# Kernel optimization log

Measured on AMD Instinct MI355X. Metric: run time of the kernel, lower is better.

The kernel has to match this reference:

```python
import jax, jax.numpy as jnp
import numpy as np

LN2 = float(np.log(2.0))
CUTOFF_L = 0.5


def _ssp(x):
    # shifted softplus: log(0.5*exp(x) + 0.5)
    return jax.nn.softplus(x) - LN2


def _pair_idx(n):
    # ordered pairs arranged [n, n-1]: for each i, all j != i
    idx = np.arange(n)
    j = np.stack([np.concatenate([idx[:k], idx[k + 1:]]) for k in range(n)])  # [n, n-1]
    i = np.broadcast_to(idx[:, None], j.shape)
    return jnp.asarray(i), jnp.asarray(j)


def _mlp3(x, w1, b1, w2, b2, w3, b3):
    h = _ssp(x @ w1 + b1)
    h = _ssp(h @ w2 + b2)
    return h @ w3 + b3


def _backflow_cutoff(r, L=CUTOFF_L):
    r = r / L
    return jnp.where(r < L, r ** 2 * (6.0 - 8.0 * r + 3.0 * r ** 2), jnp.ones((), r.dtype))


def setup_inputs() -> dict:
    key = jax.random.key(0)
    ks = jax.random.split(key, 12)
    B, N, D, K = 512, 32, 256, 8
    dims_e = [D, 40, 6, 1]
    dims_n = [D, 81, 25, 8]

    def lin(k, fi, fo):
        return jax.random.normal(k, (fi, fo), jnp.float32) / np.sqrt(fi)

    inp = {
        'rs': jax.random.normal(ks[0], (B, N, 3), jnp.float32),
        'xs': jax.random.normal(ks[1], (B, N, D), jnp.float32),
        'coords': jax.random.normal(ks[2], (K, 3), jnp.float32) * 2.0,
        'ew1': lin(ks[3], dims_e[0], dims_e[1]), 'eb1': jnp.zeros((dims_e[1],), jnp.float32),
        'ew2': lin(ks[4], dims_e[1], dims_e[2]), 'eb2': jnp.zeros((dims_e[2],), jnp.float32),
        'ew3': lin(ks[5], dims_e[2], dims_e[3]), 'eb3': jnp.zeros((dims_e[3],), jnp.float32),
        'nw1': lin(ks[6], dims_n[0], dims_n[1]), 'nb1': jnp.zeros((dims_n[1],), jnp.float32),
        'nw2': lin(ks[7], dims_n[1], dims_n[2]), 'nb2': jnp.zeros((dims_n[2],), jnp.float32),
        'nw3': lin(ks[8], dims_n[2], dims_n[3]), 'nb3': jnp.zeros((dims_n[3],), jnp.float32),
    }
    return inp


def reference(rs, xs, coords, ew1, eb1, ew2, eb2, ew3, eb3,
              nw1, nb1, nw2, nb2, nw3, nb3):
    n_elec = rs.shape[-2]
    i, j = _pair_idx(n_elec)  # [n, n-1] static index arrays

    # electron-electron backflow
    diffs_elec = rs[..., i, :] - rs[..., j, :]                    # [B, n, n-1, 3]
    pair_feat = xs[..., i, :] * xs[..., j, :]                     # [B, n, n-1, D]
    w_pair = _mlp3(pair_feat, ew1, eb1, ew2, eb2, ew3, eb3)       # [B, n, n-1, 1]
    bf_elec = (w_pair * diffs_elec).sum(axis=-2)                  # [B, n, 3]

    # electron-nucleus backflow
    diffs_nuc = rs[..., :, None, :] - coords                      # [B, n, K, 3]
    w_nuc = _mlp3(xs, nw1, nb1, nw2, nb2, nw3, nb3)               # [B, n, K]
    bf_nuc = (w_nuc[..., None] * diffs_nuc).sum(axis=-2)          # [B, n, 3]

    dist_nuc = jnp.linalg.norm(diffs_nuc, axis=-1)                # [B, n, K]
    cutoff = _backflow_cutoff(dist_nuc).prod(axis=-1)             # [B, n]

    return rs + 1e-4 * cutoff[..., None] * (bf_elec + bf_nuc)
```

## Files before the change

kernel.cpp:

```cpp
#include <hip/hip_runtime.h>
#include <stdint.h>

static constexpr int B_ = 512, N_ = 32, D_ = 256, K_ = 8;
static constexpr int E1 = 40, E2 = 6;
static constexpr int N1 = 81, N2 = 25, N3 = 8;
static constexpr int XBP = 264;
static constexpr int H1P = 72;
static constexpr int HEP = 96;
static constexpr int EWT = 264;
static constexpr int TKP = 48;
static constexpr int NWP = 104;
static constexpr int TILE16 = 16 * TKP;
static constexpr float LN2f  = 0.69314718055994530942f;
static constexpr float L2Ef  = 1.44269504088896340736f;

typedef float    f32x4 __attribute__((ext_vector_type(4)));
typedef _Float16 f16x8 __attribute__((ext_vector_type(8)));

__device__ __forceinline__ float sspf(float x) {
    float t = __builtin_amdgcn_exp2f(x * L2Ef);
    return LN2f * __builtin_amdgcn_logf(fmaf(t, 0.5f, 0.5f));
}

__global__ __launch_bounds__(512) void k_fused(
    const float* __restrict__ rs, const float* __restrict__ xs,
    const float* __restrict__ coords,
    const float* __restrict__ ew1, const float* __restrict__ eb1,
    const float* __restrict__ ew2, const float* __restrict__ eb2,
    const float* __restrict__ ew3, const float* __restrict__ eb3,
    const float* __restrict__ nw1, const float* __restrict__ nb1,
    const float* __restrict__ nw2, const float* __restrict__ nb2,
    const float* __restrict__ nw3, const float* __restrict__ nb3,
    float* __restrict__ out)
{
    __shared__ alignas(16) _Float16 xs_h[N_ * XBP];
    __shared__ alignas(16) _Float16 wbuf[E1 * EWT];
    __shared__ alignas(16) char uni[18688];
    __shared__ float nw3_s[N2 * N3];
    __shared__ float rs_s[N_ * 3];
    __shared__ float nb2_s[N2];
    __shared__ float nb3_s[N3];
    __shared__ float co_s[K_ * 3];
    __shared__ float bfn_s[N_ * 3];
    __shared__ float cut_s[N_];
    __shared__ float bfe_s[N_ * 3];

    _Float16* h1e  = (_Float16*)(uni + 9216);
    float*    h2e  = (float*)(uni + 15360);
    _Float16* nw2T = (_Float16*)uni;

    const int b = blockIdx.x, t = threadIdx.x;
    const int wv = t >> 6, l = t & 63, quad = l >> 4, c = l & 15;

    f16x8 b2f[2];
    #pragma unroll
    for (int Kt = 0; Kt < 2; ++Kt) {
        union { uint32_t d[4]; f16x8 v; } f;
        #pragma unroll
        for (int d2 = 0; d2 < 4; ++d2) {
            int k0 = Kt * 32 + quad * 8 + 2 * d2;
            union { _Float16 h[2]; uint32_t u; } pk;
            pk.h[0] = (_Float16)((k0 < E1 && c < E2) ? ew2[k0 * E2 + c] : 0.f);
            pk.h[1] = (_Float16)((k0 + 1 < E1 && c < E2) ? ew2[(k0 + 1) * E2 + c] : 0.f);
            f.d[d2] = pk.u;
        }
        b2f[Kt] = f.v;
    }
    float eb1v[3];
    #pragma unroll
    for (int Nt = 0; Nt < 3; ++Nt) { int n = Nt * 16 + c; eb1v[Nt] = (n < E1) ? eb1[n] : 0.f; }
    const float eb2v = (c < E2) ? eb2[c] : 0.f;
    const float w3v  = (c < E2) ? ew3[c] : 0.f;
    const float eb3v = eb3[0];

    {
        const float4* src = (const float4*)(xs + (size_t)b * N_ * D_);
        #pragma unroll
        for (int u = 0; u < 4; ++u) {
            int q = t + 512 * u;
            float4 v = src[q];
            int row = q >> 6, col4 = q & 63;
            union { _Float16 h[4]; uint64_t u64; } pk;
            pk.h[0] = (_Float16)v.x; pk.h[1] = (_Float16)v.y;
            pk.h[2] = (_Float16)v.z; pk.h[3] = (_Float16)v.w;
            *(uint64_t*)&xs_h[row * XBP + col4 * 4] = pk.u64;
        }
    }
    {
        const float4* src = (const float4*)ew1;
        #pragma unroll
        for (int u = 0; u < 5; ++u) {
            int q = t + 512 * u;
            float4 v = src[q];
            int k = q / 10, n0 = (q - 10 * k) * 4;
            wbuf[(n0 + 0) * EWT + k] = (_Float16)v.x;
            wbuf[(n0 + 1) * EWT + k] = (_Float16)v.y;
            wbuf[(n0 + 2) * EWT + k] = (_Float16)v.z;
            wbuf[(n0 + 3) * EWT + k] = (_Float16)v.w;
        }
    }
    if (t < 128) {
        int m = t >> 2, q4 = t & 3;
        *(uint64_t*)(uni + 9216 + m * (HEP * 2) + 160 + q4 * 8) = 0ull;
    }
    if (t < N_ * 3) rs_s[t] = rs[b * N_ * 3 + t];
    if (t < N2 * N3) nw3_s[t] = nw3[t];
    if (t < N2) nb2_s[t] = nb2[t];
    if (t < N3) nb3_s[t] = nb3[t];
    if (t < K_ * 3) co_s[t] = coords[t];
    __syncthreads();

    if (wv < 6) {
        _Float16* tile = (_Float16*)uni + wv * TILE16;
        const int ln = l & 15, lq = l >> 4;
        const int gn = wv * 16 + ln;
        const bool gok = (gn < N1);
        const int n_col = wv * 16 + c;
        const float nb1v = (n_col < N1) ? nb1[n_col] : 0.f;

        float pf[8];
        #pragma unroll
        for (int u = 0; u < 8; ++u)
            pf[u] = gok ? nw1[(lq + 4 * u) * N1 + gn] : 0.f;

        f32x4 acc[2];
        acc[0] = (f32x4){0.f, 0.f, 0.f, 0.f};
        acc[1] = (f32x4){0.f, 0.f, 0.f, 0.f};

        #pragma unroll 1
        for (int Kt = 0; Kt < 8; ++Kt) {
            #pragma unroll
            for (int u = 0; u < 8; ++u)
                tile[ln * TKP + lq + 4 * u] = (_Float16)pf[u];
            if (Kt < 7) {
                const float* wk = nw1 + (Kt + 1) * 32 * N1 + gn;
                #pragma unroll
                for (int u = 0; u < 8; ++u)
                    pf[u] = gok ? wk[(lq + 4 * u) * N1] : 0.f;
            }
            f16x8 Bf = *(const f16x8*)&tile[c * TKP + quad * 8];
            #pragma unroll
            for (int Mt = 0; Mt < 2; ++Mt) {
                f16x8 A = *(const f16x8*)&xs_h[(Mt * 16 + c) * XBP + Kt * 32 + quad * 8];
                acc[Mt] = __builtin_amdgcn_mfma_f32_16x16x32_f16(A, Bf, acc[Mt], 0, 0, 0);
            }
        }
        if (n_col < N1) {
            #pragma unroll
            for (int Mt = 0; Mt < 2; ++Mt)
                #pragma unroll
                for (int r2 = 0; r2 < 4; ++r2) {
                    int m = Mt * 16 + quad * 4 + r2;
                    h1e[m * HEP + n_col] = (_Float16)sspf(acc[Mt][r2] + nb1v);
                }
        }
    }
    __syncthreads();

    f16x8 b1f[3][8];
    #pragma unroll
    for (int Nt = 0; Nt < 3; ++Nt) {
        int n = Nt * 16 + c;
        bool ok = (n < E1);
        int row = ok ? n : 0;
        #pragma unroll
        for (int Kt = 0; Kt < 8; ++Kt) {
            f16x8 v = *(const f16x8*)&wbuf[row * EWT + Kt * 32 + quad * 8];
            if (!ok) v = (f16x8)(_Float16)0.f;
            b1f[Nt][Kt] = v;
        }
    }
    #pragma unroll
    for (int u = 0; u < 6; ++u) {
        int idx = t + 512 * u;
        int n = idx / 96, kk = idx - 96 * n;
        float v = (kk < N1 && n < N2) ? nw2[kk * N2 + n] : 0.f;
        nw2T[n * NWP + kk] = (_Float16)v;
    }
    __syncthreads();

    if (wv < 4) {
        const int Mt = wv & 1, Nt = wv >> 1;
        f32x4 acc2 = {0.f, 0.f, 0.f, 0.f};
        #pragma unroll
        for (int Kt2 = 0; Kt2 < 3; ++Kt2) {
            f16x8 A  = *(const f16x8*)&h1e[(Mt * 16 + c) * HEP + Kt2 * 32 + quad * 8];
            f16x8 Bf = *(const f16x8*)&nw2T[(Nt * 16 + c) * NWP + Kt2 * 32 + quad * 8];
            acc2 = __builtin_amdgcn_mfma_f32_16x16x32_f16(A, Bf, acc2, 0, 0, 0);
        }
        int n = Nt * 16 + c;
        if (n < N2) {
            #pragma unroll
            for (int r2 = 0; r2 < 4; ++r2) {
                int m = Mt * 16 + quad * 4 + r2;
                h2e[m * 26 + n] = sspf(acc2[r2] + nb2_s[n]);
            }
        }
    }
    __syncthreads();

    if (t < 256) {
        const int r = t >> 3, s = t & 7;
        float w = nb3_s[s];
        const int rb = r * 26;
        #pragma unroll
        for (int kk = 0; kk < N2; ++kk)
            w = fmaf(h2e[rb + kk], nw3_s[kk * N3 + s], w);

        float dx = rs_s[r * 3 + 0] - co_s[s * 3 + 0];
        float dy = rs_s[r * 3 + 1] - co_s[s * 3 + 1];
        float dz = rs_s[r * 3 + 2] - co_s[s * 3 + 2];
        float cx = w * dx, cy = w * dy, cz = w * dz;
        #pragma unroll
        for (int m2 = 1; m2 < 8; m2 <<= 1) {
            cx += __shfl_xor(cx, m2);
            cy += __shfl_xor(cy, m2);
            cz += __shfl_xor(cz, m2);
        }
        float rr  = sqrtf(dx * dx + dy * dy + dz * dz);
        float xsc = 2.f * rr;
        float cf  = (xsc < 0.5f) ? xsc * xsc * (6.f - 8.f * xsc + 3.f * xsc * xsc) : 1.f;
        #pragma unroll
        for (int m2 = 1; m2 < 8; m2 <<= 1) cf *= __shfl_xor(cf, m2);
        if (s == 0) {
            bfn_s[r * 3 + 0] = cx;
            bfn_s[r * 3 + 1] = cy;
            bfn_s[r * 3 + 2] = cz;
            cut_s[r] = cf;
        }
    }
    __syncthreads();

    _Float16* myh1 = (_Float16*)(uni + wv * (16 * H1P * 2));
    *(uint64_t*)&myh1[c * H1P + 48 + quad * 4] = 0ull;

    #pragma unroll 1
    for (int q8 = 0; q8 < 4; ++q8) {
        const int i = wv + 8 * q8;
        f32x4 acc[2][3];
        #pragma unroll
        for (int h = 0; h < 2; ++h)
            #pragma unroll
            for (int Nt = 0; Nt < 3; ++Nt) acc[h][Nt] = (f32x4){0.f, 0.f, 0.f, 0.f};

        #pragma unroll
        for (int Kt = 0; Kt < 8; ++Kt) {
            const int koff = Kt * 32 + quad * 8;
            f16x8 iv  = *(const f16x8*)&xs_h[i * XBP + koff];
            f16x8 jv0 = *(const f16x8*)&xs_h[c * XBP + koff];
            f16x8 jv1 = *(const f16x8*)&xs_h[(16 + c) * XBP + koff];
            f16x8 A0 = iv * jv0;
            f16x8 A1 = iv * jv1;
            #pragma unroll
            for (int Nt = 0; Nt < 3; ++Nt) {
                acc[0][Nt] = __builtin_amdgcn_mfma_f32_16x16x32_f16(A0, b1f[Nt][Kt], acc[0][Nt], 0, 0, 0);
                acc[1][Nt] = __builtin_amdgcn_mfma_f32_16x16x32_f16(A1, b1f[Nt][Kt], acc[1][Nt], 0, 0, 0);
            }
        }

        const float rix = rs_s[i * 3 + 0], riy = rs_s[i * 3 + 1], riz = rs_s[i * 3 + 2];
        float cxi = 0.f, cyi = 0.f, czi = 0.f;
        #pragma unroll
        for (int h = 0; h < 2; ++h) {
            #pragma unroll
            for (int Nt = 0; Nt < 3; ++Nt) {
                #pragma unroll
                for (int r2 = 0; r2 < 4; ++r2) {
                    float hv = sspf(acc[h][Nt][r2] + eb1v[Nt]);
                    myh1[(quad * 4 + r2) * H1P + Nt * 16 + c] = (_Float16)hv;
                }
            }
            f32x4 acc2 = {0.f, 0.f, 0.f, 0.f};
            #pragma unroll
            for (int Kt2 = 0; Kt2 < 2; ++Kt2) {
                f16x8 a2 = *(const f16x8*)&myh1[c * H1P + Kt2 * 32 + quad * 8];
                acc2 = __builtin_amdgcn_mfma_f32_16x16x32_f16(a2, b2f[Kt2], acc2, 0, 0, 0);
            }
            float wp[4];
            #pragma unroll
            for (int r2 = 0; r2 < 4; ++r2) wp[r2] = sspf(acc2[r2] + eb2v) * w3v;
            #pragma unroll
            for (int m2 = 1; m2 < 16; m2 <<= 1) {
                #pragma unroll
                for (int r2 = 0; r2 < 4; ++r2) wp[r2] += __shfl_xor(wp[r2], m2);
            }
            #pragma unroll
            for (int r2 = 0; r2 < 4; ++r2) {
                int j = quad * 4 + r2 + 16 * h;
                float wj = wp[r2] + eb3v;
                cxi = fmaf(wj, rix - rs_s[j * 3 + 0], cxi);
                cyi = fmaf(wj, riy - rs_s[j * 3 + 1], cyi);
                czi = fmaf(wj, riz - rs_s[j * 3 + 2], czi);
            }
        }
        #pragma unroll
        for (int m2 = 16; m2 < 64; m2 <<= 1) {
            cxi += __shfl_xor(cxi, m2);
            cyi += __shfl_xor(cyi, m2);
            czi += __shfl_xor(czi, m2);
        }
        if (l == 0) {
            bfe_s[i * 3 + 0] = cxi;
            bfe_s[i * 3 + 1] = cyi;
            bfe_s[i * 3 + 2] = czi;
        }
    }
    __syncthreads();

    if (t < N_ * 3) {
        int i = t / 3;
        out[(size_t)b * (N_ * 3) + t] =
            rs_s[t] + 1e-4f * cut_s[i] * (bfe_s[t] + bfn_s[t]);
    }
}

extern "C" void kernel_launch(void* const* d_in, const int* in_sizes, int n_in,
                              void* d_out, int out_size, void* d_ws, size_t ws_size,
                              hipStream_t stream)
{
    const float* rs     = (const float*)d_in[0];
    const float* xs     = (const float*)d_in[1];
    const float* coords = (const float*)d_in[2];
    const float* ew1    = (const float*)d_in[3];
    const float* eb1    = (const float*)d_in[4];
    const float* ew2    = (const float*)d_in[5];
    const float* eb2    = (const float*)d_in[6];
    const float* ew3    = (const float*)d_in[7];
    const float* eb3    = (const float*)d_in[8];
    const float* nw1    = (const float*)d_in[9];
    const float* nb1    = (const float*)d_in[10];
    const float* nw2    = (const float*)d_in[11];
    const float* nb2    = (const float*)d_in[12];
    const float* nw3    = (const float*)d_in[13];
    const float* nb3    = (const float*)d_in[14];

    k_fused<<<B_, 512, 0, stream>>>(rs, xs, coords, ew1, eb1, ew2, eb2, ew3, eb3,
                                    nw1, nb1, nw2, nb2, nw3, nb3, (float*)d_out);
}
```

Baseline: 133.8 us.

## Transpose edge MLP MFMAs to chain layers in registers and fold log2 scaling

The edge-MLP first-layer MFMA now has its operands swapped, so each lane's accumulator holds hidden units for one pair column. That output can feed the second layer directly as a 16x16x16 MFMA B-operand, with no LDS round trip through a per-wave h1 buffer. The ln2/log2e factors of the shifted softplus are folded into weights and biases, so each activation skips two multiplies. Biases are preloaded into the accumulators, and the final reduction becomes two cross-quad shuffles. The barrier before the pair loop and the LDS staging are removed, at the cost of slightly different fp16 rounding from the scaled weights.

```diff
diff --git a/kernel.cpp b/kernel.cpp
--- a/kernel.cpp
+++ b/kernel.cpp
@@ -5,7 +5,6 @@
 static constexpr int E1 = 40, E2 = 6;
 static constexpr int N1 = 81, N2 = 25, N3 = 8;
 static constexpr int XBP = 264;
-static constexpr int H1P = 72;
 static constexpr int HEP = 96;
 static constexpr int EWT = 264;
 static constexpr int TKP = 48;
@@ -16,10 +15,17 @@
 
 typedef float    f32x4 __attribute__((ext_vector_type(4)));
 typedef _Float16 f16x8 __attribute__((ext_vector_type(8)));
-
-__device__ __forceinline__ float sspf(float x) {
-    float t = __builtin_amdgcn_exp2f(x * L2Ef);
-    return LN2f * __builtin_amdgcn_logf(fmaf(t, 0.5f, 0.5f));
+typedef _Float16 f16x4 __attribute__((ext_vector_type(4)));
+
+#if __has_builtin(__builtin_amdgcn_mfma_f32_16x16x16_f16)
+#define MFMA16(A, B, C) __builtin_amdgcn_mfma_f32_16x16x16_f16((A), (B), (C), 0, 0, 0)
+#else
+#define MFMA16(A, B, C) __builtin_amdgcn_mfma_f32_16x16x16f16((A), (B), (C), 0, 0, 0)
+#endif
+
+__device__ __forceinline__ float ssp2(float t) {
+    float e = __builtin_amdgcn_exp2f(t);
+    return __builtin_amdgcn_logf(fmaf(e, 0.5f, 0.5f));
 }
 
 __global__ __launch_bounds__(512) void k_fused(
@@ -44,6 +50,8 @@
     __shared__ float bfn_s[N_ * 3];
     __shared__ float cut_s[N_];
     __shared__ float bfe_s[N_ * 3];
+    __shared__ alignas(16) float eb1_s[48];
+    __shared__ alignas(16) float b2_s[16];
 
     _Float16* h1e  = (_Float16*)(uni + 9216);
     float*    h2e  = (float*)(uni + 15360);
@@ -52,25 +60,23 @@
     const int b = blockIdx.x, t = threadIdx.x;
     const int wv = t >> 6, l = t & 63, quad = l >> 4, c = l & 15;
 
-    f16x8 b2f[2];
+    f16x4 b2fT[3];
     #pragma unroll
-    for (int Kt = 0; Kt < 2; ++Kt) {
-        union { uint32_t d[4]; f16x8 v; } f;
-        #pragma unroll
-        for (int d2 = 0; d2 < 4; ++d2) {
-            int k0 = Kt * 32 + quad * 8 + 2 * d2;
-            union { _Float16 h[2]; uint32_t u; } pk;
-            pk.h[0] = (_Float16)((k0 < E1 && c < E2) ? ew2[k0 * E2 + c] : 0.f);
-            pk.h[1] = (_Float16)((k0 + 1 < E1 && c < E2) ? ew2[(k0 + 1) * E2 + c] : 0.f);
-            f.d[d2] = pk.u;
-        }
-        b2f[Kt] = f.v;
-    }
-    float eb1v[3];
+    for (int Nt = 0; Nt < 3; ++Nt) {
+        f16x4 p;
+        #pragma unroll
+        for (int r = 0; r < 4; ++r) {
+            int n = Nt * 16 + quad * 4 + r;
+            p[r] = (_Float16)((n < E1 && c < E2) ? ew2[n * E2 + c] : 0.f);
+        }
+        b2fT[Nt] = p;
+    }
+    float w3q[4];
     #pragma unroll
-    for (int Nt = 0; Nt < 3; ++Nt) { int n = Nt * 16 + c; eb1v[Nt] = (n < E1) ? eb1[n] : 0.f; }
-    const float eb2v = (c < E2) ? eb2[c] : 0.f;
-    const float w3v  = (c < E2) ? ew3[c] : 0.f;
+    for (int r = 0; r < 4; ++r) {
+        int m = quad * 4 + r;
+        w3q[r] = (m < E2) ? ew3[m] * LN2f : 0.f;
+    }
     const float eb3v = eb3[0];
 
     {
@@ -93,10 +99,10 @@
             int q = t + 512 * u;
             float4 v = src[q];
             int k = q / 10, n0 = (q - 10 * k) * 4;
-            wbuf[(n0 + 0) * EWT + k] = (_Float16)v.x;
-            wbuf[(n0 + 1) * EWT + k] = (_Float16)v.y;
-            wbuf[(n0 + 2) * EWT + k] = (_Float16)v.z;
-            wbuf[(n0 + 3) * EWT + k] = (_Float16)v.w;
+            wbuf[(n0 + 0) * EWT + k] = (_Float16)(v.x * L2Ef);
+            wbuf[(n0 + 1) * EWT + k] = (_Float16)(v.y * L2Ef);
+            wbuf[(n0 + 2) * EWT + k] = (_Float16)(v.z * L2Ef);
+            wbuf[(n0 + 3) * EWT + k] = (_Float16)(v.w * L2Ef);
         }
     }
     if (t < 128) {
@@ -104,10 +110,12 @@
         *(uint64_t*)(uni + 9216 + m * (HEP * 2) + 160 + q4 * 8) = 0ull;
     }
     if (t < N_ * 3) rs_s[t] = rs[b * N_ * 3 + t];
-    if (t < N2 * N3) nw3_s[t] = nw3[t];
-    if (t < N2) nb2_s[t] = nb2[t];
+    if (t < N2 * N3) nw3_s[t] = nw3[t] * LN2f;
+    if (t < N2) nb2_s[t] = nb2[t] * L2Ef;
     if (t < N3) nb3_s[t] = nb3[t];
     if (t < K_ * 3) co_s[t] = coords[t];
+    if (t < 48) eb1_s[t] = (t < E1) ? eb1[t] * L2Ef : 0.f;
+    if (t < 16) b2_s[t] = (t < E2) ? eb2[t] * L2Ef : 0.f;
     __syncthreads();
 
     if (wv < 6) {
@@ -116,7 +124,7 @@
         const int gn = wv * 16 + ln;
         const bool gok = (gn < N1);
         const int n_col = wv * 16 + c;
-        const float nb1v = (n_col < N1) ? nb1[n_col] : 0.f;
+        const float nb1v = (n_col < N1) ? nb1[n_col] * L2Ef : 0.f;
 
         float pf[8];
         #pragma unroll
@@ -131,7 +139,7 @@
         for (int Kt = 0; Kt < 8; ++Kt) {
             #pragma unroll
             for (int u = 0; u < 8; ++u)
-                tile[ln * TKP + lq + 4 * u] = (_Float16)pf[u];
+                tile[ln * TKP + lq + 4 * u] = (_Float16)(pf[u] * L2Ef);
             if (Kt < 7) {
                 const float* wk = nw1 + (Kt + 1) * 32 * N1 + gn;
                 #pragma unroll
@@ -151,7 +159,7 @@
                 #pragma unroll
                 for (int r2 = 0; r2 < 4; ++r2) {
                     int m = Mt * 16 + quad * 4 + r2;
-                    h1e[m * HEP + n_col] = (_Float16)sspf(acc[Mt][r2] + nb1v);
+                    h1e[m * HEP + n_col] = (_Float16)ssp2(acc[Mt][r2] + nb1v);
                 }
         }
     }
@@ -193,7 +201,7 @@
             #pragma unroll
             for (int r2 = 0; r2 < 4; ++r2) {
                 int m = Mt * 16 + quad * 4 + r2;
-                h2e[m * 26 + n] = sspf(acc2[r2] + nb2_s[n]);
+                h2e[m * 26 + n] = ssp2(acc2[r2] + nb2_s[n]);
             }
         }
     }
@@ -229,19 +237,17 @@
             cut_s[r] = cf;
         }
     }
-    __syncthreads();
-
-    _Float16* myh1 = (_Float16*)(uni + wv * (16 * H1P * 2));
-    *(uint64_t*)&myh1[c * H1P + 48 + quad * 4] = 0ull;
 
     #pragma unroll 1
     for (int q8 = 0; q8 < 4; ++q8) {
         const int i = wv + 8 * q8;
         f32x4 acc[2][3];
         #pragma unroll
-        for (int h = 0; h < 2; ++h)
-            #pragma unroll
-            for (int Nt = 0; Nt < 3; ++Nt) acc[h][Nt] = (f32x4){0.f, 0.f, 0.f, 0.f};
+        for (int Nt = 0; Nt < 3; ++Nt) {
+            f32x4 bias = *(const f32x4*)&eb1_s[Nt * 16 + quad * 4];
+            acc[0][Nt] = bias;
+            acc[1][Nt] = bias;
+        }
 
         #pragma unroll
         for (int Kt = 0; Kt < 8; ++Kt) {
@@ -249,52 +255,43 @@
             f16x8 iv  = *(const f16x8*)&xs_h[i * XBP + koff];
             f16x8 jv0 = *(const f16x8*)&xs_h[c * XBP + koff];
             f16x8 jv1 = *(const f16x8*)&xs_h[(16 + c) * XBP + koff];
-            f16x8 A0 = iv * jv0;
-            f16x8 A1 = iv * jv1;
+            f16x8 P0 = iv * jv0;
+            f16x8 P1 = iv * jv1;
             #pragma unroll
             for (int Nt = 0; Nt < 3; ++Nt) {
-                acc[0][Nt] = __builtin_amdgcn_mfma_f32_16x16x32_f16(A0, b1f[Nt][Kt], acc[0][Nt], 0, 0, 0);
-                acc[1][Nt] = __builtin_amdgcn_mfma_f32_16x16x32_f16(A1, b1f[Nt][Kt], acc[1][Nt], 0, 0, 0);
+                acc[0][Nt] = __builtin_amdgcn_mfma_f32_16x16x32_f16(b1f[Nt][Kt], P0, acc[0][Nt], 0, 0, 0);
+                acc[1][Nt] = __builtin_amdgcn_mfma_f32_16x16x32_f16(b1f[Nt][Kt], P1, acc[1][Nt], 0, 0, 0);
             }
         }
 
         const float rix = rs_s[i * 3 + 0], riy = rs_s[i * 3 + 1], riz = rs_s[i * 3 + 2];
         float cxi = 0.f, cyi = 0.f, czi = 0.f;
+        const f32x4 b2i = *(const f32x4*)&b2_s[quad * 4];
         #pragma unroll
         for (int h = 0; h < 2; ++h) {
+            f32x4 acc2 = b2i;
             #pragma unroll
             for (int Nt = 0; Nt < 3; ++Nt) {
+                f16x4 bh;
                 #pragma unroll
-                for (int r2 = 0; r2 < 4; ++r2) {
-                    float hv = sspf(acc[h][Nt][r2] + eb1v[Nt]);
-                    myh1[(quad * 4 + r2) * H1P + Nt * 16 + c] = (_Float16)hv;
-                }
-            }
-            f32x4 acc2 = {0.f, 0.f, 0.f, 0.f};
-            #pragma unroll
-            for (int Kt2 = 0; Kt2 < 2; ++Kt2) {
-                f16x8 a2 = *(const f16x8*)&myh1[c * H1P + Kt2 * 32 + quad * 8];
-                acc2 = __builtin_amdgcn_mfma_f32_16x16x32_f16(a2, b2f[Kt2], acc2, 0, 0, 0);
-            }
-            float wp[4];
-            #pragma unroll
-            for (int r2 = 0; r2 < 4; ++r2) wp[r2] = sspf(acc2[r2] + eb2v) * w3v;
-            #pragma unroll
-            for (int m2 = 1; m2 < 16; m2 <<= 1) {
-                #pragma unroll
-                for (int r2 = 0; r2 < 4; ++r2) wp[r2] += __shfl_xor(wp[r2], m2);
-            }
-            #pragma unroll
-            for (int r2 = 0; r2 < 4; ++r2) {
-                int j = quad * 4 + r2 + 16 * h;
-                float wj = wp[r2] + eb3v;
-                cxi = fmaf(wj, rix - rs_s[j * 3 + 0], cxi);
-                cyi = fmaf(wj, riy - rs_s[j * 3 + 1], cyi);
-                czi = fmaf(wj, riz - rs_s[j * 3 + 2], czi);
-            }
-        }
-        #pragma unroll
-        for (int m2 = 16; m2 < 64; m2 <<= 1) {
+                for (int r2 = 0; r2 < 4; ++r2)
+                    bh[r2] = (_Float16)ssp2(acc[h][Nt][r2]);
+                acc2 = MFMA16(b2fT[Nt], bh, acc2);
+            }
+            float ws = 0.f;
+            #pragma unroll
+            for (int r2 = 0; r2 < 4; ++r2)
+                ws = fmaf(w3q[r2], ssp2(acc2[r2]), ws);
+            ws += __shfl_xor(ws, 16);
+            ws += __shfl_xor(ws, 32);
+            float wj = ws + eb3v;
+            int j = c + 16 * h;
+            cxi = fmaf(wj, rix - rs_s[j * 3 + 0], cxi);
+            cyi = fmaf(wj, riy - rs_s[j * 3 + 1], cyi);
+            czi = fmaf(wj, riz - rs_s[j * 3 + 2], czi);
+        }
+        #pragma unroll
+        for (int m2 = 1; m2 < 16; m2 <<= 1) {
             cxi += __shfl_xor(cxi, m2);
             cyi += __shfl_xor(cyi, m2);
             czi += __shfl_xor(czi, m2);
```

After: 127.6 us. 4.7% less time.
